# Kernel tuning notes

Hardware: AMD Instinct MI355X
Metric: run time of the kernel (lower is better)

Reference implementation:

```python
import jax, jax.numpy as jnp
import numpy as np
import math

D_SINGLE, D_PAIR, H, PQ, PV = 384, 128, 12, 4, 8
DH = D_SINGLE // H
OUT_DIM = H * DH + H * PV * 4 + H * D_PAIR


def setup_inputs() -> dict:
    key = jax.random.key(0)
    ks = jax.random.split(key, 24)
    B, L = 1, 512
    inp = {
        'single': jax.random.normal(ks[0], (B, L, D_SINGLE), jnp.float32),
        'pair': jax.random.normal(ks[1], (B, L, L, D_PAIR), jnp.float32),
        'rot_mats': jax.random.normal(ks[2], (B, L, 3, 3), jnp.float32),
        'trans': jax.random.normal(ks[3], (B, L, 3), jnp.float32),
        'mask': jnp.ones((B, L), jnp.float32),
        'ln_w': jnp.ones((D_SINGLE,), jnp.float32),
        'ln_b': jnp.zeros((D_SINGLE,), jnp.float32),
        'Wq': jax.random.normal(ks[4], (D_SINGLE, H * DH), jnp.float32) * 0.02,
        'bq': jnp.zeros((H * DH,), jnp.float32),
        'Wk': jax.random.normal(ks[5], (D_SINGLE, H * DH), jnp.float32) * 0.02,
        'bk': jnp.zeros((H * DH,), jnp.float32),
        'Wv': jax.random.normal(ks[6], (D_SINGLE, H * DH), jnp.float32) * 0.02,
        'bv': jnp.zeros((H * DH,), jnp.float32),
        'Wqp': jax.random.normal(ks[7], (D_SINGLE, H * PQ * 3), jnp.float32) * 0.02,
        'bqp': jnp.zeros((H * PQ * 3,), jnp.float32),
        'Wkp': jax.random.normal(ks[8], (D_SINGLE, H * PQ * 3), jnp.float32) * 0.02,
        'bkp': jnp.zeros((H * PQ * 3,), jnp.float32),
        'Wvp': jax.random.normal(ks[9], (D_SINGLE, H * PV * 3), jnp.float32) * 0.02,
        'bvp': jnp.zeros((H * PV * 3,), jnp.float32),
        'Wpb': jax.random.normal(ks[10], (D_PAIR, H), jnp.float32) * 0.02,
        'bpb': jnp.zeros((H,), jnp.float32),
        'Wo': jax.random.normal(ks[11], (OUT_DIM, D_SINGLE), jnp.float32) * 0.02,
        'bo': jnp.zeros((D_SINGLE,), jnp.float32),
        'w_c': jnp.asarray(1.0 / math.sqrt(3.0), jnp.float32),
        'w_l': jnp.asarray(1.0 / 3.0, jnp.float32),
        'gamma_h': jnp.ones((H,), jnp.float32),
    }
    return inp


def _layer_norm(x, w, b, eps=1e-5):
    mu = jnp.mean(x, axis=-1, keepdims=True)
    var = jnp.mean((x - mu) ** 2, axis=-1, keepdims=True)
    return (x - mu) * jax.lax.rsqrt(var + eps) * w + b


def reference(single, pair, rot_mats, trans, mask, ln_w, ln_b, Wq, bq, Wk, bk, Wv, bv,
              Wqp, bqp, Wkp, bkp, Wvp, bvp, Wpb, bpb, Wo, bo, w_c, w_l, gamma_h):
    B, L, _ = single.shape
    sn = _layer_norm(single, ln_w, ln_b)
    q = (sn @ Wq + bq).reshape(B, L, H, DH)
    k = (sn @ Wk + bk).reshape(B, L, H, DH)
    v = (sn @ Wv + bv).reshape(B, L, H, DH)
    qp = (sn @ Wqp + bqp).reshape(B, L, H, PQ, 3)
    kp = (sn @ Wkp + bkp).reshape(B, L, H, PQ, 3)
    vp = (sn @ Wvp + bvp).reshape(B, L, H, PV, 3)

    t = trans[:, :, None, None, :]  # [B,L,1,1,3]
    qg = jnp.einsum('blij,blhpj->blhpi', rot_mats, qp) + t
    kg = jnp.einsum('blij,blhpj->blhpi', rot_mats, kp) + t
    vg = jnp.einsum('blij,blhpj->blhpi', rot_mats, vp) + t

    # sequence logits [B,H,L,L]
    seq_logits = jnp.einsum('bihd,bjhd->bhij', q, k) * w_c / math.sqrt(DH)

    # geometric logits: pairwise point distances [B,H,L,L]
    q_pts = jnp.transpose(qg, (0, 2, 1, 3, 4))  # [B,H,L,PQ,3]
    k_pts = jnp.transpose(kg, (0, 2, 1, 3, 4))
    diff = q_pts[:, :, :, None] - k_pts[:, :, None]  # [B,H,L,L,PQ,3]
    dist_sq = jnp.sum(diff ** 2, axis=-1)            # [B,H,L,L,PQ]
    geo_logits = -0.5 * jnp.sum(dist_sq, axis=-1) * gamma_h[None, :, None, None] * w_l

    pair_bias = jnp.transpose(pair @ Wpb + bpb, (0, 3, 1, 2))  # [B,H,L,L]
    logits = seq_logits + geo_logits + pair_bias

    mask_2d = (mask[:, :, None] * mask[:, None, :])[:, None]  # [B,1,L,L]
    logits = jnp.where(mask_2d > 0, logits, jnp.float32(-1e9))
    attn = jax.nn.softmax(logits, axis=-1)  # [B,H,L,L]

    # sequence aggregation -> [B,L,H,DH]
    seq_out = jnp.einsum('bhij,bjhd->bihd', attn, v).reshape(B, L, H * DH)

    # point aggregation -> local frame features
    pts_out = jnp.einsum('bhij,bjhpd->bihpd', attn, vg)  # [B,L,H,PV,3]
    pts_local = jnp.einsum('blji,blhpj->blhpi', rot_mats, pts_out - t)
    pts_norm = jnp.linalg.norm(pts_local, axis=-1, keepdims=True)
    pts_feat = jnp.concatenate([pts_norm, pts_local], axis=-1).reshape(B, L, H * PV * 4)

    # pair aggregation -> [B,L,H*D_PAIR]
    pair_out = jnp.einsum('bhij,bijd->bihd', attn, pair).reshape(B, L, H * D_PAIR)

    combined = jnp.concatenate([seq_out, pts_feat, pair_out], axis=-1)
    return combined @ Wo + bo
```

## Files before the change

kernel.cpp:

```cpp
#include <hip/hip_runtime.h>
#include <math.h>

#define LQ    512
#define DS    384
#define DPAIR 128
#define NH    12
#define NPP   1792
#define TJC   64
#define NC    8

typedef unsigned short u16;
typedef unsigned int   u32;
typedef __attribute__((ext_vector_type(8))) short bf16x8;
typedef __attribute__((ext_vector_type(4))) float f32x4;

__device__ inline u16 bf16_rne(float x) {
  u32 u = __float_as_uint(x);
  u32 r = (u + 0x7FFFu + ((u >> 16) & 1u)) >> 16;
  return (u16)r;
}
__device__ inline void split_bf16(float x, u16& h, u16& l) {
  u16 hb = bf16_rne(x);
  float hf = __uint_as_float(((u32)hb) << 16);
  h = hb;
  l = bf16_rne(x - hf);
}

__global__ __launch_bounds__(256) void k_prep(
    const float* __restrict__ Wq, const float* __restrict__ Wk,
    const float* __restrict__ Wv, const float* __restrict__ Wqp,
    const float* __restrict__ Wkp, const float* __restrict__ Wvp,
    const float* __restrict__ bq, const float* __restrict__ bk,
    const float* __restrict__ bv, const float* __restrict__ bqp,
    const float* __restrict__ bkp, const float* __restrict__ bvp,
    const float* __restrict__ Wpb, const float* __restrict__ Wo,
    const float* __restrict__ xs, const float* __restrict__ ln_w,
    const float* __restrict__ ln_b,
    u16* __restrict__ Wth, u16* __restrict__ Wtl,
    float* __restrict__ bcat, float* __restrict__ WpbT,
    u16* __restrict__ WoTh, u16* __restrict__ WoTl,
    u16* __restrict__ snh, u16* __restrict__ snl) {
  __shared__ u16 sh_hi[64][66], sh_lo[64][66];
  int blk = blockIdx.x, t = threadIdx.x;
  if (blk < 168) {
    int kb = blk / 28, cb = blk % 28;
    int k0 = kb * 64, c0 = cb * 64;
    for (int e = t; e < 4096; e += 256) {
      int rr = e >> 6, cc = e & 63;
      int k = k0 + rr, c = c0 + cc;
      float v = 0.f;
      if (c < 384)       v = Wq[k*384 + c];
      else if (c < 768)  v = Wk[k*384 + c-384];
      else if (c < 1152) v = Wv[k*384 + c-768];
      else if (c < 1296) v = Wqp[k*144 + c-1152];
      else if (c < 1440) v = Wkp[k*144 + c-1296];
      else if (c < 1728) v = Wvp[k*288 + c-1440];
      u16 h_, l_; split_bf16(v, h_, l_);
      sh_hi[rr][cc] = h_; sh_lo[rr][cc] = l_;
    }
    __syncthreads();
    for (int e = t; e < 4096; e += 256) {
      int cc = e >> 6, kk = e & 63;
      Wth[(size_t)(c0+cc)*DS + k0 + kk] = sh_hi[kk][cc];
      Wtl[(size_t)(c0+cc)*DS + k0 + kk] = sh_lo[kk][cc];
    }
  } else if (blk == 168) {
    for (int e = t; e < NPP + NH*DPAIR; e += 256) {
      if (e < NPP) {
        int c = e;
        float v = 0.f;
        if (c < 384)       v = bq[c];
        else if (c < 768)  v = bk[c-384];
        else if (c < 1152) v = bv[c-768];
        else if (c < 1296) v = bqp[c-1152];
        else if (c < 1440) v = bkp[c-1296];
        else if (c < 1728) v = bvp[c-1440];
        bcat[c] = v;
      } else {
        int e2 = e - NPP;
        int k = e2 / NH, h = e2 % NH;
        WpbT[h*DPAIR + k] = Wpb[e2];
      }
    }
  } else if (blk < 385) {
    int idx = blk - 169;
    int kt = idx % 36, nt = idx / 36;
    int k0 = kt * 64, n0 = nt * 64;
    for (int e = t; e < 4096; e += 256) {
      int rr = e >> 6, cc = e & 63;
      float v = Wo[(size_t)(k0+rr)*384 + n0 + cc];
      u16 h_, l_; split_bf16(v, h_, l_);
      sh_hi[rr][cc] = h_; sh_lo[rr][cc] = l_;
    }
    __syncthreads();
    for (int e = t; e < 4096; e += 256) {
      int cc = e >> 6, kk = e & 63;
      WoTh[(size_t)(n0+cc)*2304 + k0 + kk] = sh_hi[kk][cc];
      WoTl[(size_t)(n0+cc)*2304 + k0 + kk] = sh_lo[kk][cc];
    }
  } else {
    int i = blk - 385;
    float* red = (float*)&sh_hi[0][0];
    float a0 = xs[i*DS + t];
    float a1 = (t < 128) ? xs[i*DS + 256 + t] : 0.f;
    red[t] = a0 + a1; __syncthreads();
    for (int s = 128; s > 0; s >>= 1) { if (t < s) red[t] += red[t+s]; __syncthreads(); }
    float mu = red[0] * (1.f/384.f);
    __syncthreads();
    float d0 = a0 - mu, d1 = (t < 128) ? (a1 - mu) : 0.f;
    red[t] = d0*d0 + d1*d1; __syncthreads();
    for (int s = 128; s > 0; s >>= 1) { if (t < s) red[t] += red[t+s]; __syncthreads(); }
    float rstd = rsqrtf(red[0] * (1.f/384.f) + 1e-5f);
    u16 h_, l_;
    float y0 = d0*rstd*ln_w[t] + ln_b[t];
    split_bf16(y0, h_, l_); snh[i*DS + t] = h_; snl[i*DS + t] = l_;
    if (t < 128) {
      float y1 = d1*rstd*ln_w[256+t] + ln_b[256+t];
      split_bf16(y1, h_, l_); snh[i*DS + 256 + t] = h_; snl[i*DS + 256 + t] = l_;
    }
  }
}

__global__ __launch_bounds__(256) void k_gemm_mfma(
    const u16* __restrict__ Ah, const u16* __restrict__ Al,
    const u16* __restrict__ Bth, const u16* __restrict__ Btl,
    const float* __restrict__ bias, float* __restrict__ C,
    float* __restrict__ Cpart, int M, int N, int K) {
  int t = threadIdx.x;
  int lane = t & 63, wave = t >> 6;
  int wr = wave >> 1, wc = wave & 1;
  int i0 = blockIdx.y * 64 + wr * 32;
  int j0 = blockIdx.x * 64 + wc * 32;
  int KS = gridDim.z;
  int kper = K / KS;
  size_t kbeg = (size_t)blockIdx.z * kper;
  int lr = lane & 15, lk = (lane >> 4) << 3;

  const u16* a0h = Ah  + (size_t)(i0 + lr) * K + kbeg + lk;
  const u16* a1h = a0h + (size_t)16 * K;
  const u16* a0l = Al  + (size_t)(i0 + lr) * K + kbeg + lk;
  const u16* a1l = a0l + (size_t)16 * K;
  const u16* b0h = Bth + (size_t)(j0 + lr) * K + kbeg + lk;
  const u16* b1h = b0h + (size_t)16 * K;
  const u16* b0l = Btl + (size_t)(j0 + lr) * K + kbeg + lk;
  const u16* b1l = b0l + (size_t)16 * K;

  f32x4 c00 = {0.f,0.f,0.f,0.f}, c01 = c00, c10 = c00, c11 = c00;
  for (int k = 0; k < kper; k += 32) {
    bf16x8 A0h = *(const bf16x8*)(a0h + k);
    bf16x8 A1h = *(const bf16x8*)(a1h + k);
    bf16x8 B0h = *(const bf16x8*)(b0h + k);
    bf16x8 B1h = *(const bf16x8*)(b1h + k);
    bf16x8 A0l = *(const bf16x8*)(a0l + k);
    bf16x8 A1l = *(const bf16x8*)(a1l + k);
    bf16x8 B0l = *(const bf16x8*)(b0l + k);
    bf16x8 B1l = *(const bf16x8*)(b1l + k);
    c00 = __builtin_amdgcn_mfma_f32_16x16x32_bf16(A0h, B0h, c00, 0, 0, 0);
    c01 = __builtin_amdgcn_mfma_f32_16x16x32_bf16(A0h, B1h, c01, 0, 0, 0);
    c10 = __builtin_amdgcn_mfma_f32_16x16x32_bf16(A1h, B0h, c10, 0, 0, 0);
    c11 = __builtin_amdgcn_mfma_f32_16x16x32_bf16(A1h, B1h, c11, 0, 0, 0);
    c00 = __builtin_amdgcn_mfma_f32_16x16x32_bf16(A0h, B0l, c00, 0, 0, 0);
    c01 = __builtin_amdgcn_mfma_f32_16x16x32_bf16(A0h, B1l, c01, 0, 0, 0);
    c10 = __builtin_amdgcn_mfma_f32_16x16x32_bf16(A1h, B0l, c10, 0, 0, 0);
    c11 = __builtin_amdgcn_mfma_f32_16x16x32_bf16(A1h, B1l, c11, 0, 0, 0);
    c00 = __builtin_amdgcn_mfma_f32_16x16x32_bf16(A0l, B0h, c00, 0, 0, 0);
    c01 = __builtin_amdgcn_mfma_f32_16x16x32_bf16(A0l, B1h, c01, 0, 0, 0);
    c10 = __builtin_amdgcn_mfma_f32_16x16x32_bf16(A1l, B0h, c10, 0, 0, 0);
    c11 = __builtin_amdgcn_mfma_f32_16x16x32_bf16(A1l, B1h, c11, 0, 0, 0);
  }

  int orow = (lane >> 4) << 2;
  int col0 = j0 + lr, col1 = j0 + 16 + lr;
  if (KS == 1) {
    float bb0 = bias[col0], bb1 = bias[col1];
    #pragma unroll
    for (int r = 0; r < 4; r++) {
      int row0 = i0 + orow + r, row1 = row0 + 16;
      C[(size_t)row0*N + col0] = c00[r] + bb0;
      C[(size_t)row0*N + col1] = c01[r] + bb1;
      C[(size_t)row1*N + col0] = c10[r] + bb0;
      C[(size_t)row1*N + col1] = c11[r] + bb1;
    }
  } else {
    float* dst = Cpart + (size_t)blockIdx.z * M * N;
    #pragma unroll
    for (int r = 0; r < 4; r++) {
      int row0 = i0 + orow + r, row1 = row0 + 16;
      dst[(size_t)row0*N + col0] = c00[r];
      dst[(size_t)row0*N + col1] = c01[r];
      dst[(size_t)row1*N + col0] = c10[r];
      dst[(size_t)row1*N + col1] = c11[r];
    }
  }
}

__global__ void k_reduce_bias(const float* __restrict__ part, const float* __restrict__ bias,
                              float* __restrict__ out, int MN, int N, int KS) {
  int e = blockIdx.x * 256 + threadIdx.x;
  if (e >= MN) return;
  float s = bias[e % N];
  for (int z = 0; z < KS; z++) s += part[(size_t)z*MN + e];
  out[e] = s;
}

__global__ __launch_bounds__(256) void k_feat_logits(
    const float* __restrict__ C1, const float* __restrict__ rot,
    const float* __restrict__ trans, const float* __restrict__ gamma,
    const float* __restrict__ w_c, const float* __restrict__ w_l,
    float* __restrict__ S) {
  __shared__ u16 Ash[64][72], Asl[64][72], Bsh[64][72], Bsl[64][72];
  int h = blockIdx.z;
  int i0 = blockIdx.y * 64, j0 = blockIdx.x * 64;
  int t = threadIdx.x;

  if (t < 128) {
    int row = t & 63, side = t >> 6;
    int gi = (side ? j0 : i0) + row;
    float R[9], tr[3];
    #pragma unroll
    for (int r = 0; r < 9; r++) R[r] = rot[(size_t)gi*9 + r];
    #pragma unroll
    for (int r = 0; r < 3; r++) tr[r] = trans[(size_t)gi*3 + r];
    float sc = w_c[0] * rsqrtf(32.f);
    float gp = gamma[h] * w_l[0];
    u16 (*Fh)[72] = side ? Bsh : Ash;
    u16 (*Fl)[72] = side ? Bsl : Asl;
    const float* qk = C1 + (size_t)gi*NPP + (side ? 384 : 0) + h*32;
    u16 h_, l_;
    #pragma unroll 8
    for (int d = 0; d < 32; d++) {
      float v = side ? qk[d] : sc*qk[d];
      split_bf16(v, h_, l_); Fh[row][d] = h_; Fl[row][d] = l_;
    }
    const float* pp = C1 + (size_t)gi*NPP + (side ? 1296 : 1152) + h*12;
    float ss = 0.f;
    #pragma unroll
    for (int p = 0; p < 4; p++) {
      float x = pp[p*3], y = pp[p*3+1], z = pp[p*3+2];
      #pragma unroll
      for (int r = 0; r < 3; r++) {
        float g = fmaf(R[r*3],x, fmaf(R[r*3+1],y, fmaf(R[r*3+2],z, tr[r])));
        float v = side ? g : gp*g;
        split_bf16(v, h_, l_); Fh[row][32+p*3+r] = h_; Fl[row][32+p*3+r] = l_;
        ss = fmaf(g,g,ss);
      }
    }
    float c44 = side ? 1.f : -0.5f*gp*ss;
    float c45 = side ? -0.5f*gp*ss : 1.f;
    split_bf16(c44, h_, l_); Fh[row][44] = h_; Fl[row][44] = l_;
    split_bf16(c45, h_, l_); Fh[row][45] = h_; Fl[row][45] = l_;
    #pragma unroll
    for (int d = 46; d < 64; d++) { Fh[row][d] = 0; Fl[row][d] = 0; }
  }
  __syncthreads();

  int lane = t & 63, wave = t >> 6, wr = wave >> 1, wc = wave & 1;
  int lr = lane & 15, lk = (lane >> 4) << 3;
  f32x4 c00 = {0.f,0.f,0.f,0.f}, c01 = c00, c10 = c00, c11 = c00;
  #pragma unroll
  for (int ks = 0; ks < 64; ks += 32) {
    bf16x8 A0h = *(const bf16x8*)&Ash[wr*32 + lr][ks + lk];
    bf16x8 A1h = *(const bf16x8*)&Ash[wr*32 + 16 + lr][ks + lk];
    bf16x8 B0h = *(const bf16x8*)&Bsh[wc*32 + lr][ks + lk];
    bf16x8 B1h = *(const bf16x8*)&Bsh[wc*32 + 16 + lr][ks + lk];
    bf16x8 A0l = *(const bf16x8*)&Asl[wr*32 + lr][ks + lk];
    bf16x8 A1l = *(const bf16x8*)&Asl[wr*32 + 16 + lr][ks + lk];
    bf16x8 B0l = *(const bf16x8*)&Bsl[wc*32 + lr][ks + lk];
    bf16x8 B1l = *(const bf16x8*)&Bsl[wc*32 + 16 + lr][ks + lk];
    c00 = __builtin_amdgcn_mfma_f32_16x16x32_bf16(A0h, B0h, c00, 0, 0, 0);
    c01 = __builtin_amdgcn_mfma_f32_16x16x32_bf16(A0h, B1h, c01, 0, 0, 0);
    c10 = __builtin_amdgcn_mfma_f32_16x16x32_bf16(A1h, B0h, c10, 0, 0, 0);
    c11 = __builtin_amdgcn_mfma_f32_16x16x32_bf16(A1h, B1h, c11, 0, 0, 0);
    c00 = __builtin_amdgcn_mfma_f32_16x16x32_bf16(A0h, B0l, c00, 0, 0, 0);
    c01 = __builtin_amdgcn_mfma_f32_16x16x32_bf16(A0h, B1l, c01, 0, 0, 0);
    c10 = __builtin_amdgcn_mfma_f32_16x16x32_bf16(A1h, B0l, c10, 0, 0, 0);
    c11 = __builtin_amdgcn_mfma_f32_16x16x32_bf16(A1h, B1l, c11, 0, 0, 0);
    c00 = __builtin_amdgcn_mfma_f32_16x16x32_bf16(A0l, B0h, c00, 0, 0, 0);
    c01 = __builtin_amdgcn_mfma_f32_16x16x32_bf16(A0l, B1h, c01, 0, 0, 0);
    c10 = __builtin_amdgcn_mfma_f32_16x16x32_bf16(A1l, B0h, c10, 0, 0, 0);
    c11 = __builtin_amdgcn_mfma_f32_16x16x32_bf16(A1l, B1h, c11, 0, 0, 0);
  }

  int orow = (lane >> 4) << 2;
  int col0 = j0 + wc*32 + lr, col1 = col0 + 16;
  int rbase = i0 + wr*32 + orow;
  #pragma unroll
  for (int r = 0; r < 4; r++) {
    S[((size_t)h*LQ + rbase + r)*LQ + col0]      = c00[r];
    S[((size_t)h*LQ + rbase + r)*LQ + col1]      = c01[r];
    S[((size_t)h*LQ + rbase + 16 + r)*LQ + col0] = c10[r];
    S[((size_t)h*LQ + rbase + 16 + r)*LQ + col1] = c11[r];
  }
}

__global__ __launch_bounds__(256) void k_pair(
    const float* __restrict__ pair, const float* __restrict__ WpbT,
    const float* __restrict__ bpb, const float* __restrict__ mask,
    float* S, float* __restrict__ scs_g,
    u16* __restrict__ combh, u16* __restrict__ combl) {
  __shared__ float tile[TJC*133];
  __shared__ float wt[NH*TJC];
  __shared__ float msc[NC][NH], ssc[NC][NH];
  __shared__ float rfac[NH], dinv[NH];
  int i = blockIdx.x, t = threadIdx.x;
  int j = t & 63;
  int hg = t >> 6;
  int h0 = hg * 3;
  int dg = t & 31, strip = t >> 5, jb = strip*8;

  float b0 = bpb[h0], b1 = bpb[h0+1], b2 = bpb[h0+2];
  float mi = mask[i];
  const float* w0p = WpbT + (size_t)(h0+0)*DPAIR;
  const float* w1p = WpbT + (size_t)(h0+1)*DPAIR;
  const float* w2p = WpbT + (size_t)(h0+2)*DPAIR;

  float4 acc[NH];
  #pragma unroll
  for (int h = 0; h < NH; h++) acc[h] = make_float4(0.f,0.f,0.f,0.f);
  float mrun[3] = {-3.0e38f, -3.0e38f, -3.0e38f};

  float4 pf[8];
  {
    const float4* src = (const float4*)(pair + (size_t)i*LQ*DPAIR);
    #pragma unroll
    for (int u = 0; u < 8; u++) pf[u] = src[t + u*256];
  }
  #pragma unroll
  for (int u = 0; u < 8; u++) {
    int e = t + u*256; int row = e >> 5, c4 = e & 31;
    *(float4*)&tile[row*133 + c4*4] = pf[u];
  }
  __syncthreads();

  for (int c = 0; c < NC; c++) {
    if (c < NC-1) {
      const float4* src = (const float4*)(pair + ((size_t)i*LQ + (c+1)*TJC)*DPAIR);
      #pragma unroll
      for (int u = 0; u < 8; u++) pf[u] = src[t + u*256];
    }
    int j0 = c*TJC;
    float l0 = S[((size_t)(h0+0)*LQ + i)*LQ + j0 + j] + b0;
    float l1 = S[((size_t)(h0+1)*LQ + i)*LQ + j0 + j] + b1;
    float l2 = S[((size_t)(h0+2)*LQ + i)*LQ + j0 + j] + b2;
    {
      float a0 = 0.f, a1 = 0.f, a2 = 0.f;
      #pragma unroll 8
      for (int k = 0; k < DPAIR; k += 4) {
        float4 pv = *(const float4*)&tile[j*133 + k];
        float4 w0 = *(const float4*)(w0p + k);
        float4 w1 = *(const float4*)(w1p + k);
        float4 w2 = *(const float4*)(w2p + k);
        a0 = fmaf(pv.x,w0.x, fmaf(pv.y,w0.y, fmaf(pv.z,w0.z, fmaf(pv.w,w0.w, a0))));
        a1 = fmaf(pv.x,w1.x, fmaf(pv.y,w1.y, fmaf(pv.z,w1.z, fmaf(pv.w,w1.w, a1))));
        a2 = fmaf(pv.x,w2.x, fmaf(pv.y,w2.y, fmaf(pv.z,w2.z, fmaf(pv.w,w2.w, a2))));
      }
      l0 += a0; l1 += a1; l2 += a2;
      bool dead = (mi * mask[j0 + j] <= 0.f);
      if (dead) { l0 = -1e9f; l1 = -1e9f; l2 = -1e9f; }
    }
    #pragma unroll
    for (int q = 0; q < 3; q++) {
      float lv = (q==0) ? l0 : (q==1) ? l1 : l2;
      float m = lv;
      #pragma unroll
      for (int o = 32; o > 0; o >>= 1) m = fmaxf(m, __shfl_xor(m, o, 64));
      float w = __expf(lv - m);
      float sm = w;
      #pragma unroll
      for (int o = 32; o > 0; o >>= 1) sm += __shfl_xor(sm, o, 64);
      float mnew = fmaxf(mrun[q], m);
      float f  = __expf(m - mnew);
      float rf = __expf(mrun[q] - mnew);
      mrun[q] = mnew;
      wt[(h0+q)*TJC + j] = w * f;
      S[((size_t)(h0+q)*LQ + i)*LQ + j0 + j] = w;
      if (j == 0) { msc[c][h0+q] = m; ssc[c][h0+q] = sm; rfac[h0+q] = rf; }
    }
    __syncthreads();
    {
      float4 pv[8];
      #pragma unroll
      for (int q = 0; q < 8; q++) pv[q] = *(const float4*)&tile[(jb+q)*133 + dg*4];
      #pragma unroll
      for (int h = 0; h < NH; h++) {
        float rf = rfac[h];
        float4 w0 = *(const float4*)&wt[h*TJC + jb];
        float4 w1 = *(const float4*)&wt[h*TJC + jb + 4];
        float wq[8] = {w0.x,w0.y,w0.z,w0.w,w1.x,w1.y,w1.z,w1.w};
        float4 a = acc[h];
        a.x *= rf; a.y *= rf; a.z *= rf; a.w *= rf;
        #pragma unroll
        for (int q = 0; q < 8; q++) {
          a.x = fmaf(wq[q], pv[q].x, a.x);
          a.y = fmaf(wq[q], pv[q].y, a.y);
          a.z = fmaf(wq[q], pv[q].z, a.z);
          a.w = fmaf(wq[q], pv[q].w, a.w);
        }
        acc[h] = a;
      }
    }
    __syncthreads();
    if (c < NC-1) {
      #pragma unroll
      for (int u = 0; u < 8; u++) {
        int e = t + u*256; int row = e >> 5, c4 = e & 31;
        *(float4*)&tile[row*133 + c4*4] = pf[u];
      }
      __syncthreads();
    }
  }

  if (j == 0) {
    #pragma unroll
    for (int q = 0; q < 3; q++) {
      float M = mrun[q];
      float den = 0.f;
      #pragma unroll
      for (int c = 0; c < NC; c++) den += ssc[c][h0+q] * __expf(msc[c][h0+q] - M);
      float inv = 1.f / den;
      dinv[h0+q] = inv;
      #pragma unroll
      for (int c = 0; c < NC; c++)
        scs_g[((size_t)i*NH + h0+q)*NC + c] = __expf(msc[c][h0+q] - M) * inv;
    }
  }

  float4* red4 = (float4*)tile;
  float4 tot[2];
  tot[0] = make_float4(0.f,0.f,0.f,0.f);
  tot[1] = make_float4(0.f,0.f,0.f,0.f);
  #pragma unroll
  for (int half = 0; half < 2; half++) {
    if ((strip >> 2) == half) {
      #pragma unroll
      for (int h = 0; h < NH; h++)
        red4[(((strip & 3)*NH) + h)*32 + dg] = acc[h];
    }
    __syncthreads();
    for (int e = t, u = 0; e < NH*32; e += 256, u++) {
      int rh = e >> 5, rd = e & 31;
      #pragma unroll
      for (int s4 = 0; s4 < 4; s4++) {
        float4 v = red4[((s4*NH) + rh)*32 + rd];
        tot[u].x += v.x; tot[u].y += v.y; tot[u].z += v.z; tot[u].w += v.w;
      }
    }
    __syncthreads();
  }
  for (int e = t, u = 0; e < NH*32; e += 256, u++) {
    int rh = e >> 5, rd = e & 31;
    float inv = dinv[rh];
    size_t dst = (size_t)i*2304 + 768 + rh*DPAIR + rd*4;
    u16 h_, l_;
    split_bf16(tot[u].x * inv, h_, l_); combh[dst+0] = h_; combl[dst+0] = l_;
    split_bf16(tot[u].y * inv, h_, l_); combh[dst+1] = h_; combl[dst+1] = l_;
    split_bf16(tot[u].z * inv, h_, l_); combh[dst+2] = h_; combl[dst+2] = l_;
    split_bf16(tot[u].w * inv, h_, l_); combh[dst+3] = h_; combl[dst+3] = l_;
  }
}

__global__ __launch_bounds__(256, 2) void k_attn_full(
    const float* __restrict__ S, const float* __restrict__ scs_g,
    const float* __restrict__ C1, const float* __restrict__ rot,
    const float* __restrict__ trans,
    u16* __restrict__ combh, u16* __restrict__ combl) {
  __shared__ u16 Ash[64][72], Asl[64][72], Vsh[64][72], Vsl[64][72];
  __shared__ float scs_l[64][NC];
  __shared__ float Of[64][66];
  int i0 = blockIdx.x * 64;
  int h = blockIdx.y;
  int t = threadIdx.x, lane = t & 63, wave = t >> 6, wr = wave >> 1, wc = wave & 1;
  int lr = lane & 15, lk = (lane >> 4) << 3;

  if (t < 64) {
    #pragma unroll
    for (int c = 0; c < NC; c++)
      scs_l[t][c] = scs_g[((size_t)(i0+t)*NH + h)*NC + c];
  }
  __syncthreads();

  f32x4 c00 = {0.f,0.f,0.f,0.f}, c01 = c00, c10 = c00, c11 = c00;
  for (int jc = 0; jc < 8; jc++) {
    int j0 = jc * 64;
    for (int e = t; e < 4096; e += 256) {
      int m = e >> 6, j = e & 63;
      float w = S[((size_t)h*LQ + i0 + m)*LQ + j0 + j] * scs_l[m][jc];
      u16 h_, l_; split_bf16(w, h_, l_);
      Ash[m][j] = h_; Asl[m][j] = l_;
    }
    {
      int j = t & 63, ng = t >> 6;
      int gj = j0 + j;
      u16 h_, l_;
      if (ng < 2) {
        const float* vrow = C1 + (size_t)gj*NPP + 768 + h*32 + ng*16;
        #pragma unroll
        for (int q = 0; q < 16; q++) {
          split_bf16(vrow[q], h_, l_);
          Vsh[ng*16 + q][j] = h_; Vsl[ng*16 + q][j] = l_;
        }
      } else {
        const float* prow = C1 + (size_t)gj*NPP + 1440 + h*24;
        const float* R = rot + (size_t)gj*9;
        const float* tr = trans + (size_t)gj*3;
        int nbase = ng * 16;
        #pragma unroll
        for (int q = 0; q < 16; q++) {
          int n = nbase + q;
          float val = 0.f;
          if (n < 56) {
            int pp = (n - 32) / 3, rr = (n - 32) % 3;
            float x = prow[pp*3], y = prow[pp*3+1], z = prow[pp*3+2];
            val = fmaf(R[rr*3], x, fmaf(R[rr*3+1], y, fmaf(R[rr*3+2], z, tr[rr])));
          }
          split_bf16(val, h_, l_);
          Vsh[n][j] = h_; Vsl[n][j] = l_;
        }
      }
    }
    __syncthreads();
    #pragma unroll
    for (int ks = 0; ks < 64; ks += 32) {
      bf16x8 A0h = *(const bf16x8*)&Ash[wr*32 + lr][ks + lk];
      bf16x8 A1h = *(const bf16x8*)&Ash[wr*32 + 16 + lr][ks + lk];
      bf16x8 B0h = *(const bf16x8*)&Vsh[wc*32 + lr][ks + lk];
      bf16x8 B1h = *(const bf16x8*)&Vsh[wc*32 + 16 + lr][ks + lk];
      bf16x8 A0l = *(const bf16x8*)&Asl[wr*32 + lr][ks + lk];
      bf16x8 A1l = *(const bf16x8*)&Asl[wr*32 + 16 + lr][ks + lk];
      bf16x8 B0l = *(const bf16x8*)&Vsl[wc*32 + lr][ks + lk];
      bf16x8 B1l = *(const bf16x8*)&Vsl[wc*32 + 16 + lr][ks + lk];
      c00 = __builtin_amdgcn_mfma_f32_16x16x32_bf16(A0h, B0h, c00, 0, 0, 0);
      c01 = __builtin_amdgcn_mfma_f32_16x16x32_bf16(A0h, B1h, c01, 0, 0, 0);
      c10 = __builtin_amdgcn_mfma_f32_16x16x32_bf16(A1h, B0h, c10, 0, 0, 0);
      c11 = __builtin_amdgcn_mfma_f32_16x16x32_bf16(A1h, B1h, c11, 0, 0, 0);
      c00 = __builtin_amdgcn_mfma_f32_16x16x32_bf16(A0h, B0l, c00, 0, 0, 0);
      c01 = __builtin_amdgcn_mfma_f32_16x16x32_bf16(A0h, B1l, c01, 0, 0, 0);
      c10 = __builtin_amdgcn_mfma_f32_16x16x32_bf16(A1h, B0l, c10, 0, 0, 0);
      c11 = __builtin_amdgcn_mfma_f32_16x16x32_bf16(A1h, B1l, c11, 0, 0, 0);
      c00 = __builtin_amdgcn_mfma_f32_16x16x32_bf16(A0l, B0h, c00, 0, 0, 0);
      c01 = __builtin_amdgcn_mfma_f32_16x16x32_bf16(A0l, B1h, c01, 0, 0, 0);
      c10 = __builtin_amdgcn_mfma_f32_16x16x32_bf16(A1l, B0h, c10, 0, 0, 0);
      c11 = __builtin_amdgcn_mfma_f32_16x16x32_bf16(A1l, B1h, c11, 0, 0, 0);
    }
    __syncthreads();
  }

  int orow = (lane >> 4) << 2;
  #pragma unroll
  for (int r = 0; r < 4; r++) {
    Of[wr*32 + orow + r][wc*32 + lr]           = c00[r];
    Of[wr*32 + orow + r][wc*32 + 16 + lr]      = c01[r];
    Of[wr*32 + 16 + orow + r][wc*32 + lr]      = c10[r];
    Of[wr*32 + 16 + orow + r][wc*32 + 16 + lr] = c11[r];
  }
  __syncthreads();

  for (int e = t; e < 64*40; e += 256) {
    int w = e % 40, m = e / 40;
    int gi = i0 + m;
    u16 h_, l_;
    if (w < 32) {
      split_bf16(Of[m][w], h_, l_);
      combh[(size_t)gi*2304 + h*32 + w] = h_;
      combl[(size_t)gi*2304 + h*32 + w] = l_;
    } else {
      int pp = w - 32;
      float g0 = Of[m][32+pp*3], g1 = Of[m][32+pp*3+1], g2 = Of[m][32+pp*3+2];
      const float* R = rot + (size_t)gi*9;
      const float* tr = trans + (size_t)gi*3;
      float x = g0 - tr[0], y = g1 - tr[1], z = g2 - tr[2];
      float lx = fmaf(R[0],x, fmaf(R[3],y, R[6]*z));
      float ly = fmaf(R[1],x, fmaf(R[4],y, R[7]*z));
      float lz = fmaf(R[2],x, fmaf(R[5],y, R[8]*z));
      float nrm = sqrtf(fmaf(lx,lx, fmaf(ly,ly, lz*lz)));
      size_t dst = (size_t)gi*2304 + 384 + ((size_t)h*8 + pp)*4;
      split_bf16(nrm, h_, l_); combh[dst+0] = h_; combl[dst+0] = l_;
      split_bf16(lx,  h_, l_); combh[dst+1] = h_; combl[dst+1] = l_;
      split_bf16(ly,  h_, l_); combh[dst+2] = h_; combl[dst+2] = l_;
      split_bf16(lz,  h_, l_); combh[dst+3] = h_; combl[dst+3] = l_;
    }
  }
}

extern "C" void kernel_launch(void* const* d_in, const int* in_sizes, int n_in,
                              void* d_out, int out_size, void* d_ws, size_t ws_size,
                              hipStream_t stream) {
  const float* single = (const float*)d_in[0];
  const float* pair   = (const float*)d_in[1];
  const float* rot    = (const float*)d_in[2];
  const float* trans  = (const float*)d_in[3];
  const float* mask   = (const float*)d_in[4];
  const float* ln_w   = (const float*)d_in[5];
  const float* ln_b   = (const float*)d_in[6];
  const float* Wq     = (const float*)d_in[7];
  const float* bq     = (const float*)d_in[8];
  const float* Wk     = (const float*)d_in[9];
  const float* bk     = (const float*)d_in[10];
  const float* Wv     = (const float*)d_in[11];
  const float* bv     = (const float*)d_in[12];
  const float* Wqp    = (const float*)d_in[13];
  const float* bqp    = (const float*)d_in[14];
  const float* Wkp    = (const float*)d_in[15];
  const float* bkp    = (const float*)d_in[16];
  const float* Wvp    = (const float*)d_in[17];
  const float* bvp    = (const float*)d_in[18];
  const float* Wpb    = (const float*)d_in[19];
  const float* bpb    = (const float*)d_in[20];
  const float* Wo     = (const float*)d_in[21];
  const float* bo     = (const float*)d_in[22];
  const float* w_c    = (const float*)d_in[23];
  const float* w_l    = (const float*)d_in[24];
  const float* gamma  = (const float*)d_in[25];
  float* out = (float*)d_out;

  float* p = (float*)d_ws;
  auto alloc = [&](size_t n) { float* r = p; p += n; return r; };
  u16* WcatTh = (u16*)alloc((size_t)NPP*DS/2);
  u16* WcatTl = (u16*)alloc((size_t)NPP*DS/2);
  u16* snh    = (u16*)alloc((size_t)LQ*DS/2);
  u16* snl    = (u16*)alloc((size_t)LQ*DS/2);
  u16* WoTh   = (u16*)alloc((size_t)DS*2304/2);
  u16* WoTl   = (u16*)alloc((size_t)DS*2304/2);
  u16* combh  = (u16*)alloc((size_t)LQ*2304/2);
  u16* combl  = (u16*)alloc((size_t)LQ*2304/2);
  float* bcat    = alloc(NPP);
  float* WpbT    = alloc((size_t)NH*DPAIR);
  float* C1      = alloc((size_t)LQ*NPP);
  float* S       = alloc((size_t)NH*LQ*LQ);
  float* scs_g   = alloc((size_t)LQ*NH*NC);
  float* outpart = alloc((size_t)8*LQ*DS);

  k_prep<<<dim3(897), 256, 0, stream>>>(
      Wq, Wk, Wv, Wqp, Wkp, Wvp, bq, bk, bv, bqp, bkp, bvp, Wpb, Wo,
      single, ln_w, ln_b, WcatTh, WcatTl, bcat, WpbT, WoTh, WoTl, snh, snl);
  k_gemm_mfma<<<dim3(NPP/64, LQ/64, 1), 256, 0, stream>>>(
      snh, snl, WcatTh, WcatTl, bcat, C1, nullptr, LQ, NPP, DS);
  k_feat_logits<<<dim3(LQ/64, LQ/64, NH), 256, 0, stream>>>(
      C1, rot, trans, gamma, w_c, w_l, S);
  k_pair<<<dim3(LQ), 256, 0, stream>>>(
      pair, WpbT, bpb, mask, S, scs_g, combh, combl);
  k_attn_full<<<dim3(LQ/64, NH), 256, 0, stream>>>(
      S, scs_g, C1, rot, trans, combh, combl);
  k_gemm_mfma<<<dim3(DS/64, LQ/64, 8), 256, 0, stream>>>(
      combh, combl, WoTh, WoTl, nullptr, nullptr, outpart, LQ, DS, 2304);
  k_reduce_bias<<<dim3((LQ*DS + 255)/256), 256, 0, stream>>>(outpart, bo, out, LQ*DS, DS, 8);
}
```

Baseline: 421.0 us.

## Double-buffer pair tiles via async LDS loads and split attention aggregation over keys

```diff
diff --git a/kernel.cpp b/kernel.cpp
--- a/kernel.cpp
+++ b/kernel.cpp
@@ -24,6 +24,12 @@
   float hf = __uint_as_float(((u32)hb) << 16);
   h = hb;
   l = bf16_rne(x - hf);
+}
+
+__device__ inline void async_copy16(const float* g, float* l) {
+  auto gp = (const __attribute__((address_space(1))) float*)(g);
+  auto lp = (__attribute__((address_space(3))) float*)(l);
+  __builtin_amdgcn_global_load_lds(gp, lp, 16, 0, 0);
 }
 
 __global__ __launch_bounds__(256) void k_prep(
@@ -293,21 +299,60 @@
   }
 }
 
+__global__ __launch_bounds__(256) void k_vt(
+    const float* __restrict__ C1, const float* __restrict__ rot,
+    const float* __restrict__ trans,
+    u16* __restrict__ Vth, u16* __restrict__ Vtl) {
+  int h = blockIdx.x;
+  int i = blockIdx.y * 256 + threadIdx.x;
+  float R[9], tr[3];
+  #pragma unroll
+  for (int r = 0; r < 9; r++) R[r] = rot[(size_t)i*9 + r];
+  #pragma unroll
+  for (int r = 0; r < 3; r++) tr[r] = trans[(size_t)i*3 + r];
+  const float* vrow = C1 + (size_t)i*NPP + 768 + h*32;
+  const float* prow = C1 + (size_t)i*NPP + 1440 + h*24;
+  u16 h_, l_;
+  #pragma unroll 8
+  for (int n = 0; n < 32; n++) {
+    split_bf16(vrow[n], h_, l_);
+    Vth[((size_t)h*64 + n)*LQ + i] = h_;
+    Vtl[((size_t)h*64 + n)*LQ + i] = l_;
+  }
+  #pragma unroll
+  for (int p = 0; p < 8; p++) {
+    float x = prow[p*3], y = prow[p*3+1], z = prow[p*3+2];
+    #pragma unroll
+    for (int r = 0; r < 3; r++) {
+      float g = fmaf(R[r*3],x, fmaf(R[r*3+1],y, fmaf(R[r*3+2],z, tr[r])));
+      split_bf16(g, h_, l_);
+      Vth[((size_t)h*64 + 32 + p*3 + r)*LQ + i] = h_;
+      Vtl[((size_t)h*64 + 32 + p*3 + r)*LQ + i] = l_;
+    }
+  }
+  #pragma unroll
+  for (int n = 56; n < 64; n++) {
+    Vth[((size_t)h*64 + n)*LQ + i] = 0;
+    Vtl[((size_t)h*64 + n)*LQ + i] = 0;
+  }
+}
+
 __global__ __launch_bounds__(256) void k_pair(
     const float* __restrict__ pair, const float* __restrict__ WpbT,
     const float* __restrict__ bpb, const float* __restrict__ mask,
     float* S, float* __restrict__ scs_g,
     u16* __restrict__ combh, u16* __restrict__ combl) {
-  __shared__ float tile[TJC*133];
+  __shared__ float tile[2][TJC*DPAIR];
   __shared__ float wt[NH*TJC];
   __shared__ float msc[NC][NH], ssc[NC][NH];
   __shared__ float rfac[NH], dinv[NH];
   int i = blockIdx.x, t = threadIdx.x;
-  int j = t & 63;
-  int hg = t >> 6;
-  int h0 = hg * 3;
+  int lane = t & 63, wave = t >> 6;
+  int j = lane;
+  int h0 = wave * 3;
   int dg = t & 31, strip = t >> 5, jb = strip*8;
 
+  const float* prow = pair + (size_t)i*LQ*DPAIR;
   float b0 = bpb[h0], b1 = bpb[h0+1], b2 = bpb[h0+2];
   float mi = mask[i];
   const float* w0p = WpbT + (size_t)(h0+0)*DPAIR;
@@ -319,25 +364,25 @@
   for (int h = 0; h < NH; h++) acc[h] = make_float4(0.f,0.f,0.f,0.f);
   float mrun[3] = {-3.0e38f, -3.0e38f, -3.0e38f};
 
-  float4 pf[8];
-  {
-    const float4* src = (const float4*)(pair + (size_t)i*LQ*DPAIR);
-    #pragma unroll
-    for (int u = 0; u < 8; u++) pf[u] = src[t + u*256];
-  }
-  #pragma unroll
-  for (int u = 0; u < 8; u++) {
-    int e = t + u*256; int row = e >> 5, c4 = e & 31;
-    *(float4*)&tile[row*133 + c4*4] = pf[u];
-  }
+  auto dma = [&](int c, int buf) {
+    #pragma unroll
+    for (int u = 0; u < 8; u++) {
+      int seg = wave*8 + u;
+      int F = seg*64 + lane;
+      int row = F >> 5, k4s = F & 31;
+      int k4 = k4s ^ (row & 7);
+      const float* src = prow + (size_t)(c*TJC + row)*DPAIR + k4*4;
+      async_copy16(src, &tile[buf][seg*256]);
+    }
+  };
+
+  dma(0, 0);
+  asm volatile("s_waitcnt vmcnt(0)" ::: "memory");
   __syncthreads();
+  int cur = 0;
 
   for (int c = 0; c < NC; c++) {
-    if (c < NC-1) {
-      const float4* src = (const float4*)(pair + ((size_t)i*LQ + (c+1)*TJC)*DPAIR);
-      #pragma unroll
-      for (int u = 0; u < 8; u++) pf[u] = src[t + u*256];
-    }
+    if (c < NC-1) dma(c+1, cur^1);
     int j0 = c*TJC;
     float l0 = S[((size_t)(h0+0)*LQ + i)*LQ + j0 + j] + b0;
     float l1 = S[((size_t)(h0+1)*LQ + i)*LQ + j0 + j] + b1;
@@ -345,11 +390,11 @@
     {
       float a0 = 0.f, a1 = 0.f, a2 = 0.f;
       #pragma unroll 8
-      for (int k = 0; k < DPAIR; k += 4) {
-        float4 pv = *(const float4*)&tile[j*133 + k];
-        float4 w0 = *(const float4*)(w0p + k);
-        float4 w1 = *(const float4*)(w1p + k);
-        float4 w2 = *(const float4*)(w2p + k);
+      for (int kk = 0; kk < 32; kk++) {
+        float4 pv = *(const float4*)&tile[cur][(j*32 + (kk ^ (j & 7)))*4];
+        float4 w0 = *(const float4*)(w0p + kk*4);
+        float4 w1 = *(const float4*)(w1p + kk*4);
+        float4 w2 = *(const float4*)(w2p + kk*4);
         a0 = fmaf(pv.x,w0.x, fmaf(pv.y,w0.y, fmaf(pv.z,w0.z, fmaf(pv.w,w0.w, a0))));
         a1 = fmaf(pv.x,w1.x, fmaf(pv.y,w1.y, fmaf(pv.z,w1.z, fmaf(pv.w,w1.w, a1))));
         a2 = fmaf(pv.x,w2.x, fmaf(pv.y,w2.y, fmaf(pv.z,w2.z, fmaf(pv.w,w2.w, a2))));
@@ -380,7 +425,10 @@
     {
       float4 pv[8];
       #pragma unroll
-      for (int q = 0; q < 8; q++) pv[q] = *(const float4*)&tile[(jb+q)*133 + dg*4];
+      for (int q = 0; q < 8; q++) {
+        int row = jb + q;
+        pv[q] = *(const float4*)&tile[cur][(row*32 + (dg ^ (row & 7)))*4];
+      }
       #pragma unroll
       for (int h = 0; h < NH; h++) {
         float rf = rfac[h];
@@ -399,15 +447,9 @@
         acc[h] = a;
       }
     }
+    asm volatile("s_waitcnt vmcnt(0)" ::: "memory");
     __syncthreads();
-    if (c < NC-1) {
-      #pragma unroll
-      for (int u = 0; u < 8; u++) {
-        int e = t + u*256; int row = e >> 5, c4 = e & 31;
-        *(float4*)&tile[row*133 + c4*4] = pf[u];
-      }
-      __syncthreads();
-    }
+    cur ^= 1;
   }
 
   if (j == 0) {
@@ -425,7 +467,7 @@
     }
   }
 
-  float4* red4 = (float4*)tile;
+  float4* red4 = (float4*)&tile[0][0];
   float4 tot[2];
   tot[0] = make_float4(0.f,0.f,0.f,0.f);
   tot[1] = make_float4(0.f,0.f,0.f,0.f);
@@ -459,126 +501,114 @@
   }
 }
 
-__global__ __launch_bounds__(256, 2) void k_attn_full(
+__global__ __launch_bounds__(256) void k_attn_mfma(
     const float* __restrict__ S, const float* __restrict__ scs_g,
-    const float* __restrict__ C1, const float* __restrict__ rot,
-    const float* __restrict__ trans,
-    u16* __restrict__ combh, u16* __restrict__ combl) {
-  __shared__ u16 Ash[64][72], Asl[64][72], Vsh[64][72], Vsl[64][72];
-  __shared__ float scs_l[64][NC];
-  __shared__ float Of[64][66];
-  int i0 = blockIdx.x * 64;
-  int h = blockIdx.y;
-  int t = threadIdx.x, lane = t & 63, wave = t >> 6, wr = wave >> 1, wc = wave & 1;
+    const u16* __restrict__ Vth, const u16* __restrict__ Vtl,
+    float* __restrict__ psum) {
+  int t = threadIdx.x;
+  int lane = t & 63, wave = t >> 6;
+  int wr = wave >> 1, wc = wave & 1;
+  int z = blockIdx.x;
+  int i0 = blockIdx.y * 64 + wr * 32;
+  int h = blockIdx.z;
+  int n0 = wc * 32;
   int lr = lane & 15, lk = (lane >> 4) << 3;
 
-  if (t < 64) {
-    #pragma unroll
-    for (int c = 0; c < NC; c++)
-      scs_l[t][c] = scs_g[((size_t)(i0+t)*NH + h)*NC + c];
-  }
-  __syncthreads();
+  const float* a0p = S + ((size_t)h*LQ + i0 + lr)*LQ + z*128 + lk;
+  const float* a1p = a0p + (size_t)16*LQ;
+  const float* s0p = scs_g + ((size_t)(i0 + lr)*NH + h)*NC + z*2;
+  const float* s1p = scs_g + ((size_t)(i0 + 16 + lr)*NH + h)*NC + z*2;
+  const u16* b0h = Vth + ((size_t)h*64 + n0 + lr)*LQ + z*128 + lk;
+  const u16* b1h = b0h + (size_t)16*LQ;
+  const u16* b0l = Vtl + ((size_t)h*64 + n0 + lr)*LQ + z*128 + lk;
+  const u16* b1l = b0l + (size_t)16*LQ;
 
   f32x4 c00 = {0.f,0.f,0.f,0.f}, c01 = c00, c10 = c00, c11 = c00;
-  for (int jc = 0; jc < 8; jc++) {
-    int j0 = jc * 64;
-    for (int e = t; e < 4096; e += 256) {
-      int m = e >> 6, j = e & 63;
-      float w = S[((size_t)h*LQ + i0 + m)*LQ + j0 + j] * scs_l[m][jc];
-      u16 h_, l_; split_bf16(w, h_, l_);
-      Ash[m][j] = h_; Asl[m][j] = l_;
-    }
-    {
-      int j = t & 63, ng = t >> 6;
-      int gj = j0 + j;
-      u16 h_, l_;
-      if (ng < 2) {
-        const float* vrow = C1 + (size_t)gj*NPP + 768 + h*32 + ng*16;
-        #pragma unroll
-        for (int q = 0; q < 16; q++) {
-          split_bf16(vrow[q], h_, l_);
-          Vsh[ng*16 + q][j] = h_; Vsl[ng*16 + q][j] = l_;
-        }
-      } else {
-        const float* prow = C1 + (size_t)gj*NPP + 1440 + h*24;
-        const float* R = rot + (size_t)gj*9;
-        const float* tr = trans + (size_t)gj*3;
-        int nbase = ng * 16;
-        #pragma unroll
-        for (int q = 0; q < 16; q++) {
-          int n = nbase + q;
-          float val = 0.f;
-          if (n < 56) {
-            int pp = (n - 32) / 3, rr = (n - 32) % 3;
-            float x = prow[pp*3], y = prow[pp*3+1], z = prow[pp*3+2];
-            val = fmaf(R[rr*3], x, fmaf(R[rr*3+1], y, fmaf(R[rr*3+2], z, tr[rr])));
-          }
-          split_bf16(val, h_, l_);
-          Vsh[n][j] = h_; Vsl[n][j] = l_;
-        }
-      }
-    }
-    __syncthreads();
-    #pragma unroll
-    for (int ks = 0; ks < 64; ks += 32) {
-      bf16x8 A0h = *(const bf16x8*)&Ash[wr*32 + lr][ks + lk];
-      bf16x8 A1h = *(const bf16x8*)&Ash[wr*32 + 16 + lr][ks + lk];
-      bf16x8 B0h = *(const bf16x8*)&Vsh[wc*32 + lr][ks + lk];
-      bf16x8 B1h = *(const bf16x8*)&Vsh[wc*32 + 16 + lr][ks + lk];
-      bf16x8 A0l = *(const bf16x8*)&Asl[wr*32 + lr][ks + lk];
-      bf16x8 A1l = *(const bf16x8*)&Asl[wr*32 + 16 + lr][ks + lk];
-      bf16x8 B0l = *(const bf16x8*)&Vsl[wc*32 + lr][ks + lk];
-      bf16x8 B1l = *(const bf16x8*)&Vsl[wc*32 + 16 + lr][ks + lk];
-      c00 = __builtin_amdgcn_mfma_f32_16x16x32_bf16(A0h, B0h, c00, 0, 0, 0);
-      c01 = __builtin_amdgcn_mfma_f32_16x16x32_bf16(A0h, B1h, c01, 0, 0, 0);
-      c10 = __builtin_amdgcn_mfma_f32_16x16x32_bf16(A1h, B0h, c10, 0, 0, 0);
-      c11 = __builtin_amdgcn_mfma_f32_16x16x32_bf16(A1h, B1h, c11, 0, 0, 0);
-      c00 = __builtin_amdgcn_mfma_f32_16x16x32_bf16(A0h, B0l, c00, 0, 0, 0);
-      c01 = __builtin_amdgcn_mfma_f32_16x16x32_bf16(A0h, B1l, c01, 0, 0, 0);
-      c10 = __builtin_amdgcn_mfma_f32_16x16x32_bf16(A1h, B0l, c10, 0, 0, 0);
-      c11 = __builtin_amdgcn_mfma_f32_16x16x32_bf16(A1h, B1l, c11, 0, 0, 0);
-      c00 = __builtin_amdgcn_mfma_f32_16x16x32_bf16(A0l, B0h, c00, 0, 0, 0);
-      c01 = __builtin_amdgcn_mfma_f32_16x16x32_bf16(A0l, B1h, c01, 0, 0, 0);
-      c10 = __builtin_amdgcn_mfma_f32_16x16x32_bf16(A1l, B0h, c10, 0, 0, 0);
-      c11 = __builtin_amdgcn_mfma_f32_16x16x32_bf16(A1l, B1h, c11, 0, 0, 0);
-    }
-    __syncthreads();
+  #pragma unroll
+  for (int k = 0; k < 128; k += 32) {
+    int cc = (k >= 64) ? 1 : 0;
+    float sc0 = s0p[cc], sc1 = s1p[cc];
+    float4 av00 = *(const float4*)(a0p + k);
+    float4 av01 = *(const float4*)(a0p + k + 4);
+    float4 av10 = *(const float4*)(a1p + k);
+    float4 av11 = *(const float4*)(a1p + k + 4);
+    float a0v[8] = {av00.x,av00.y,av00.z,av00.w,av01.x,av01.y,av01.z,av01.w};
+    float a1v[8] = {av10.x,av10.y,av10.z,av10.w,av11.x,av11.y,av11.z,av11.w};
+    bf16x8 A0h = {}, A0l = {}, A1h = {}, A1l = {};
+    #pragma unroll
+    for (int e = 0; e < 8; e++) {
+      u16 hh, ll;
+      split_bf16(a0v[e]*sc0, hh, ll);
+      A0h[e] = (short)hh; A0l[e] = (short)ll;
+      split_bf16(a1v[e]*sc1, hh, ll);
+      A1h[e] = (short)hh; A1l[e] = (short)ll;
+    }
+    bf16x8 B0h = *(const bf16x8*)(b0h + k);
+    bf16x8 B1h = *(const bf16x8*)(b1h + k);
+    bf16x8 B0l = *(const bf16x8*)(b0l + k);
+    bf16x8 B1l = *(const bf16x8*)(b1l + k);
+    c00 = __builtin_amdgcn_mfma_f32_16x16x32_bf16(A0h, B0h, c00, 0, 0, 0);
+    c01 = __builtin_amdgcn_mfma_f32_16x16x32_bf16(A0h, B1h, c01, 0, 0, 0);
+    c10 = __builtin_amdgcn_mfma_f32_16x16x32_bf16(A1h, B0h, c10, 0, 0, 0);
+    c11 = __builtin_amdgcn_mfma_f32_16x16x32_bf16(A1h, B1h, c11, 0, 0, 0);
+    c00 = __builtin_amdgcn_mfma_f32_16x16x32_bf16(A0h, B0l, c00, 0, 0, 0);
+    c01 = __builtin_amdgcn_mfma_f32_16x16x32_bf16(A0h, B1l, c01, 0, 0, 0);
+    c10 = __builtin_amdgcn_mfma_f32_16x16x32_bf16(A1h, B0l, c10, 0, 0, 0);
+    c11 = __builtin_amdgcn_mfma_f32_16x16x32_bf16(A1h, B1l, c11, 0, 0, 0);
+    c00 = __builtin_amdgcn_mfma_f32_16x16x32_bf16(A0l, B0h, c00, 0, 0, 0);
+    c01 = __builtin_amdgcn_mfma_f32_16x16x32_bf16(A0l, B1h, c01, 0, 0, 0);
+    c10 = __builtin_amdgcn_mfma_f32_16x16x32_bf16(A1l, B0h, c10, 0, 0, 0);
+    c11 = __builtin_amdgcn_mfma_f32_16x16x32_bf16(A1l, B1h, c11, 0, 0, 0);
   }
 
   int orow = (lane >> 4) << 2;
+  int col0 = n0 + lr, col1 = n0 + 16 + lr;
   #pragma unroll
   for (int r = 0; r < 4; r++) {
-    Of[wr*32 + orow + r][wc*32 + lr]           = c00[r];
-    Of[wr*32 + orow + r][wc*32 + 16 + lr]      = c01[r];
-    Of[wr*32 + 16 + orow + r][wc*32 + lr]      = c10[r];
-    Of[wr*32 + 16 + orow + r][wc*32 + 16 + lr] = c11[r];
-  }
-  __syncthreads();
-
-  for (int e = t; e < 64*40; e += 256) {
-    int w = e % 40, m = e / 40;
-    int gi = i0 + m;
-    u16 h_, l_;
-    if (w < 32) {
-      split_bf16(Of[m][w], h_, l_);
-      combh[(size_t)gi*2304 + h*32 + w] = h_;
-      combl[(size_t)gi*2304 + h*32 + w] = l_;
-    } else {
-      int pp = w - 32;
-      float g0 = Of[m][32+pp*3], g1 = Of[m][32+pp*3+1], g2 = Of[m][32+pp*3+2];
-      const float* R = rot + (size_t)gi*9;
-      const float* tr = trans + (size_t)gi*3;
-      float x = g0 - tr[0], y = g1 - tr[1], z = g2 - tr[2];
-      float lx = fmaf(R[0],x, fmaf(R[3],y, R[6]*z));
-      float ly = fmaf(R[1],x, fmaf(R[4],y, R[7]*z));
-      float lz = fmaf(R[2],x, fmaf(R[5],y, R[8]*z));
-      float nrm = sqrtf(fmaf(lx,lx, fmaf(ly,ly, lz*lz)));
-      size_t dst = (size_t)gi*2304 + 384 + ((size_t)h*8 + pp)*4;
-      split_bf16(nrm, h_, l_); combh[dst+0] = h_; combl[dst+0] = l_;
-      split_bf16(lx,  h_, l_); combh[dst+1] = h_; combl[dst+1] = l_;
-      split_bf16(ly,  h_, l_); combh[dst+2] = h_; combl[dst+2] = l_;
-      split_bf16(lz,  h_, l_); combh[dst+3] = h_; combl[dst+3] = l_;
-    }
+    int row0 = i0 + orow + r, row1 = row0 + 16;
+    psum[(((size_t)z*LQ + row0)*NH + h)*64 + col0] = c00[r];
+    psum[(((size_t)z*LQ + row0)*NH + h)*64 + col1] = c01[r];
+    psum[(((size_t)z*LQ + row1)*NH + h)*64 + col0] = c10[r];
+    psum[(((size_t)z*LQ + row1)*NH + h)*64 + col1] = c11[r];
+  }
+}
+
+__global__ void k_avpts(const float* __restrict__ psum, const float* __restrict__ rot,
+                        const float* __restrict__ trans,
+                        u16* __restrict__ combh, u16* __restrict__ combl) {
+  int idx = blockIdx.x * 256 + threadIdx.x;
+  if (idx >= LQ*NH*40) return;
+  int w = idx % 40; int ih = idx / 40; int h = ih % NH; int i = ih / NH;
+  size_t base = ((size_t)i*NH + h)*64;
+  u16 h_, l_;
+  if (w < 32) {
+    float s = 0.f;
+    for (int z = 0; z < 4; z++) s += psum[(size_t)z*LQ*NH*64 + base + w];
+    split_bf16(s, h_, l_);
+    combh[(size_t)i*2304 + h*32 + w] = h_;
+    combl[(size_t)i*2304 + h*32 + w] = l_;
+  } else {
+    int p = w - 32;
+    float g[3];
+    #pragma unroll
+    for (int r = 0; r < 3; r++) {
+      int n = 32 + p*3 + r;
+      float s = 0.f;
+      for (int z = 0; z < 4; z++) s += psum[(size_t)z*LQ*NH*64 + base + n];
+      g[r] = s;
+    }
+    const float* R = rot + (size_t)i*9;
+    const float* tr = trans + (size_t)i*3;
+    float x = g[0]-tr[0], y = g[1]-tr[1], z = g[2]-tr[2];
+    float lx = fmaf(R[0],x, fmaf(R[3],y, R[6]*z));
+    float ly = fmaf(R[1],x, fmaf(R[4],y, R[7]*z));
+    float lz = fmaf(R[2],x, fmaf(R[5],y, R[8]*z));
+    float nrm = sqrtf(fmaf(lx,lx, fmaf(ly,ly, lz*lz)));
+    size_t dst = (size_t)i*2304 + 384 + (h*8 + p)*4;
+    split_bf16(nrm, h_, l_); combh[dst+0] = h_; combl[dst+0] = l_;
+    split_bf16(lx,  h_, l_); combh[dst+1] = h_; combl[dst+1] = l_;
+    split_bf16(ly,  h_, l_); combh[dst+2] = h_; combl[dst+2] = l_;
+    split_bf16(lz,  h_, l_); combh[dst+3] = h_; combl[dst+3] = l_;
   }
 }
 
@@ -623,11 +653,14 @@
   u16* WoTl   = (u16*)alloc((size_t)DS*2304/2);
   u16* combh  = (u16*)alloc((size_t)LQ*2304/2);
   u16* combl  = (u16*)alloc((size_t)LQ*2304/2);
+  u16* Vth    = (u16*)alloc((size_t)NH*64*LQ/2);
+  u16* Vtl    = (u16*)alloc((size_t)NH*64*LQ/2);
   float* bcat    = alloc(NPP);
   float* WpbT    = alloc((size_t)NH*DPAIR);
   float* C1      = alloc((size_t)LQ*NPP);
   float* S       = alloc((size_t)NH*LQ*LQ);
   float* scs_g   = alloc((size_t)LQ*NH*NC);
+  float* psum    = alloc((size_t)4*LQ*NH*64);
   float* outpart = alloc((size_t)8*LQ*DS);
 
   k_prep<<<dim3(897), 256, 0, stream>>>(
@@ -637,10 +670,13 @@
       snh, snl, WcatTh, WcatTl, bcat, C1, nullptr, LQ, NPP, DS);
   k_feat_logits<<<dim3(LQ/64, LQ/64, NH), 256, 0, stream>>>(
       C1, rot, trans, gamma, w_c, w_l, S);
+  k_vt<<<dim3(NH, LQ/256), 256, 0, stream>>>(C1, rot, trans, Vth, Vtl);
   k_pair<<<dim3(LQ), 256, 0, stream>>>(
       pair, WpbT, bpb, mask, S, scs_g, combh, combl);
-  k_attn_full<<<dim3(LQ/64, NH), 256, 0, stream>>>(
-      S, scs_g, C1, rot, trans, combh, combl);
+  k_attn_mfma<<<dim3(4, LQ/64, NH), 256, 0, stream>>>(
+      S, scs_g, Vth, Vtl, psum);
+  k_avpts<<<dim3((LQ*NH*40 + 255)/256), 256, 0, stream>>>(
+      psum, rot, trans, combh, combl);
   k_gemm_mfma<<<dim3(DS/64, LQ/64, 8), 256, 0, stream>>>(
       combh, combl, WoTh, WoTl, nullptr, nullptr, outpart, LQ, DS, 2304);
   k_reduce_bias<<<dim3((LQ*DS + 255)/256), 256, 0, stream>>>(outpart, bo, out, LQ*DS, DS, 8);
```

Measured after the change: 376.1 us. 10.7% less time.
